# Performance work log

Hardware: AMD Instinct MI355X
Metric: run time of the kernel (lower is better)

Reference implementation:

```python
import jax, jax.numpy as jnp
import numpy as np

S, B, D, H, FF = 1024, 8, 512, 8, 2048
HD = D // H
ALPHA, BETA = 0.5, 0.5
EPS = 1e-5


def setup_inputs() -> dict:
    key = jax.random.key(0)
    ks = jax.random.split(key, 12)
    rn = lambda k, sh, sc=0.02: jax.random.normal(k, sh, dtype=jnp.float32) * sc
    ln = jnp.stack([jnp.ones(D), jnp.zeros(D), jnp.ones(D), jnp.zeros(D)]).astype(jnp.float32)
    return {
        "src": rn(ks[0], (S, B, D), 1.0),
        "src_depth": rn(ks[1], (S, B, D), 1.0),
        "pos": rn(ks[2], (S, B, D), 1.0),
        "attn_w_img": rn(ks[3], (4, D, D)),
        "attn_b_img": jnp.zeros((4, D), jnp.float32),
        "attn_w_dpt": rn(ks[4], (4, D, D)),
        "attn_b_dpt": jnp.zeros((4, D), jnp.float32),
        "ffn_w1_img": rn(ks[5], (FF, D)),
        "ffn_b1_img": jnp.zeros((FF,), jnp.float32),
        "ffn_w2_img": rn(ks[6], (D, FF)),
        "ffn_b2_img": jnp.zeros((D,), jnp.float32),
        "ffn_w1_dpt": rn(ks[7], (FF, D)),
        "ffn_b1_dpt": jnp.zeros((FF,), jnp.float32),
        "ffn_w2_dpt": rn(ks[8], (D, FF)),
        "ffn_b2_dpt": jnp.zeros((D,), jnp.float32),
        "ln_img": ln,
        "ln_dpt": ln,
    }


def _layer_norm(x, g, b):
    m = jnp.mean(x, axis=-1, keepdims=True)
    v = jnp.var(x, axis=-1, keepdims=True)  # biased, matches torch LayerNorm
    return (x - m) * jax.lax.rsqrt(v + EPS) * g + b


def _heads(t, W, b):  # [B,S,D] x [D,D] -> [B,H,S,hd]  (torch Linear: y = x W^T + b)
    y = jnp.einsum('bsd,ed->bse', t, W) + b
    return y.reshape(B, S, H, HD).transpose(0, 2, 1, 3)


def _forward(src, src_depth, pos, attn_w_img, attn_b_img, attn_w_dpt, attn_b_dpt,
             ffn_w1_img, ffn_b1_img, ffn_w2_img, ffn_b2_img,
             ffn_w1_dpt, ffn_b1_dpt, ffn_w2_dpt, ffn_b2_dpt, ln_img, ln_dpt):
    # seq-first -> batch-first
    x = src.transpose(1, 0, 2)        # [B,S,D]
    xd = src_depth.transpose(1, 0, 2)
    p = pos.transpose(1, 0, 2)
    qk_in = x + p                     # img stream: q = k = src + pos
    # depth stream: pos_depth is None in layer.forward -> no pos embed
    q = _heads(qk_in, attn_w_img[0], attn_b_img[0])
    k = _heads(qk_in, attn_w_img[1], attn_b_img[1])
    v = _heads(x, attn_w_img[2], attn_b_img[2])
    qd = _heads(xd, attn_w_dpt[0], attn_b_dpt[0])
    kd = _heads(xd, attn_w_dpt[1], attn_b_dpt[1])
    vd = _heads(xd, attn_w_dpt[2], attn_b_dpt[2])
    scale = 1.0 / np.sqrt(HD).astype(np.float32)
    a_img = jax.nn.softmax(jnp.einsum('bhld,bhsd->bhls', q, k) * scale, axis=-1)
    a_dpt = jax.nn.softmax(jnp.einsum('bhld,bhsd->bhls', qd, kd) * scale, axis=-1)
    sh_img = (1.0 - ALPHA) * a_img + ALPHA * a_dpt
    sh_dpt = (1.0 - BETA) * a_dpt + BETA * a_img
    o_img = jnp.einsum('bhls,bhsd->bhld', sh_img, v).transpose(0, 2, 1, 3).reshape(B, S, D)
    o_dpt = jnp.einsum('bhls,bhsd->bhld', sh_dpt, vd).transpose(0, 2, 1, 3).reshape(B, S, D)
    o_img = jnp.einsum('bsd,ed->bse', o_img, attn_w_img[3]) + attn_b_img[3]
    o_dpt = jnp.einsum('bsd,ed->bse', o_dpt, attn_w_dpt[3]) + attn_b_dpt[3]
    # img residual + LN + FFN + LN
    x = _layer_norm(x + o_img, ln_img[0], ln_img[1])
    ff = jnp.einsum('bsf,df->bsd',
                    jax.nn.relu(jnp.einsum('bsd,fd->bsf', x, ffn_w1_img) + ffn_b1_img),
                    ffn_w2_img) + ffn_b2_img
    x = _layer_norm(x + ff, ln_img[2], ln_img[3])
    # depth residual + LN + FFN + LN
    xd = _layer_norm(xd + o_dpt, ln_dpt[0], ln_dpt[1])
    ffd = jnp.einsum('bsf,df->bsd',
                     jax.nn.relu(jnp.einsum('bsd,fd->bsf', xd, ffn_w1_dpt) + ffn_b1_dpt),
                     ffn_w2_dpt) + ffn_b2_dpt
    xd = _layer_norm(xd + ffd, ln_dpt[2], ln_dpt[3])
    return x.transpose(1, 0, 2), xd.transpose(1, 0, 2)  # back to [S,B,D]


def reference(src, src_depth, pos, attn_w_img, attn_b_img, attn_w_dpt, attn_b_dpt,
              ffn_w1_img, ffn_b1_img, ffn_w2_img, ffn_b2_img,
              ffn_w1_dpt, ffn_b1_dpt, ffn_w2_dpt, ffn_b2_dpt, ln_img, ln_dpt):
    return _forward(src, src_depth, pos, attn_w_img, attn_b_img, attn_w_dpt, attn_b_dpt,
                    ffn_w1_img, ffn_b1_img, ffn_w2_img, ffn_b2_img,
                    ffn_w1_dpt, ffn_b1_dpt, ffn_w2_dpt, ffn_b2_dpt, ln_img, ln_dpt)
```

## Files before the change

### kernel.cpp

```cpp
#include <hip/hip_runtime.h>
#include <math.h>

#define S_  1024
#define B_  8
#define D_  512
#define H_  8
#define HD_ 64
#define FF_ 2048
#define M_  8192
#define DD_ (D_ * D_)

typedef __attribute__((ext_vector_type(8))) short short8;
typedef __attribute__((ext_vector_type(4))) float f32x4;

static __device__ __forceinline__ unsigned short f2bf(float x) {
  union { float f; unsigned int u; } v; v.f = x;
  unsigned int r = v.u + 0x7fff + ((v.u >> 16) & 1);
  return (unsigned short)(r >> 16);
}
static __device__ __forceinline__ float bf2f(unsigned short x) {
  union { unsigned int u; float f; } v; v.u = ((unsigned int)x) << 16;
  return v.f;
}
static __device__ __forceinline__ unsigned int pack_bf2(float a, float b) {
  union { float f; unsigned int u; } x, y; x.f = a; y.f = b;
  return ((x.u + 0x8000u) >> 16) | ((y.u + 0x8000u) & 0xffff0000u);
}
static __device__ __forceinline__ void gl_lds16(const unsigned short* g, unsigned short* l) {
  __builtin_amdgcn_global_load_lds((__attribute__((address_space(1))) void*)(g),
                                   (__attribute__((address_space(3))) void*)(l), 16, 0, 0);
}
static __device__ __forceinline__ int xcd_swz(int phys, int nwg) {
  int cpx = nwg >> 3;
  return (phys & 7) * cpx + (phys >> 3);
}

struct CvtJobs { const float* in[6]; unsigned short* out[6]; };
__global__ __launch_bounds__(256) void wcvt_kernel(CvtJobs j) {
  int job = blockIdx.y;
  int i = (blockIdx.x * 256 + threadIdx.x) * 4;
  float4 v = *(const float4*)(j.in[job] + i);
  unsigned short u[4] = {f2bf(v.x), f2bf(v.y), f2bf(v.z), f2bf(v.w)};
  *(uint2*)(j.out[job] + i) = *(const uint2*)u;
}

__global__ __launch_bounds__(256) void acvt_kernel(const float* __restrict__ src,
    const float* __restrict__ srcd, const float* __restrict__ pos,
    unsigned short* __restrict__ src16, unsigned short* __restrict__ srcd16,
    unsigned short* __restrict__ qkin16) {
  int job = blockIdx.y;
  int i = (blockIdx.x * 256 + threadIdx.x) * 4;
  const float* a = (job == 0) ? src : (job == 1) ? srcd : src;
  float4 v = *(const float4*)(a + i);
  if (job == 2) {
    float4 p = *(const float4*)(pos + i);
    v.x += p.x; v.y += p.y; v.z += p.z; v.w += p.w;
  }
  unsigned short* o = (job == 0) ? src16 : (job == 1) ? srcd16 : qkin16;
  unsigned short u[4] = {f2bf(v.x), f2bf(v.y), f2bf(v.z), f2bf(v.w)};
  *(uint2*)(o + i) = *(const uint2*)u;
}

static __device__ __forceinline__ void mgemm_body(
    const unsigned short* __restrict__ X, const unsigned short* __restrict__ W,
    const float* __restrict__ bias, const float* __restrict__ resf,
    const unsigned short* __restrict__ resb, unsigned short* __restrict__ Yb,
    float* __restrict__ Yf, int N, int K, int relu, int bx, int by,
    unsigned short* As, unsigned short* Bs)
{
  int tid = threadIdx.x;
  int lane = tid & 63, w = tid >> 6;
  int ml = lane & 15, g = lane >> 4;
  int wm = w >> 1, wn = w & 1;
  int m0 = by * 128, n0 = bx * 256;
  int mxs = (ml >> 1) & 3;

  int lrow = tid >> 2;
  int sg = (tid & 3) ^ ((lrow >> 1) & 3);
  const unsigned short* gA = X + (size_t)(m0 + lrow) * K + sg * 8;
  const unsigned short* gB = W + (size_t)(n0 + lrow) * K + sg * 8;
  unsigned short* lA = As + w * 512;
  unsigned short* lB = Bs + w * 512;

  f32x4 acc[4][8];
  #pragma unroll
  for (int i = 0; i < 4; i++)
    #pragma unroll
    for (int j = 0; j < 8; j++) acc[i][j] = (f32x4){0.f, 0.f, 0.f, 0.f};

  int NT = K >> 5;

  auto STAGE = [&](int buf, int kt) {
    const unsigned short* ga = gA + kt * 32;
    const unsigned short* gb = gB + kt * 32;
    unsigned short* la = lA + buf * 4096;
    unsigned short* lb = lB + buf * 8192;
    gl_lds16(ga, la);
    gl_lds16(ga + (size_t)64 * K, la + 2048);
    gl_lds16(gb, lb);
    gl_lds16(gb + (size_t)64 * K, lb + 2048);
    gl_lds16(gb + (size_t)128 * K, lb + 4096);
    gl_lds16(gb + (size_t)192 * K, lb + 6144);
  };

  STAGE(0, 0);
  __syncthreads();

  for (int kt = 0; kt < NT; kt++) {
    int cur = kt & 1;
    if (kt + 1 < NT) STAGE(cur ^ 1, kt + 1);

    const unsigned short* lAc = As + cur * 4096;
    const unsigned short* lBc = Bs + cur * 8192;
    short8 af[4], bfr[8];
    #pragma unroll
    for (int i = 0; i < 4; i++) {
      int r = wm * 64 + i * 16 + ml;
      af[i] = *(const short8*)&lAc[r * 32 + ((g ^ mxs) * 8)];
    }
    #pragma unroll
    for (int j = 0; j < 8; j++) {
      int r = wn * 128 + j * 16 + ml;
      bfr[j] = *(const short8*)&lBc[r * 32 + ((g ^ mxs) * 8)];
    }
    #pragma unroll
    for (int i = 0; i < 4; i++)
      #pragma unroll
      for (int j = 0; j < 8; j++)
        acc[i][j] = __builtin_amdgcn_mfma_f32_16x16x32_bf16(af[i], bfr[j], acc[i][j], 0, 0, 0);

    __syncthreads();
  }

  #pragma unroll
  for (int i = 0; i < 4; i++) {
    int grow = m0 + wm * 64 + i * 16 + g * 4;
    #pragma unroll
    for (int j = 0; j < 8; j++) {
      int gcol = n0 + wn * 128 + j * 16 + ml;
      float bv = bias[gcol];
      #pragma unroll
      for (int r = 0; r < 4; r++) {
        size_t idx = (size_t)(grow + r) * N + gcol;
        float v = acc[i][j][r] + bv;
        if (resf) v += resf[idx];
        if (resb) v += bf2f(resb[idx]);
        if (relu) v = fmaxf(v, 0.0f);
        if (Yb) Yb[idx] = f2bf(v);
        if (Yf) Yf[idx] = v;
      }
    }
  }
}

__global__ __launch_bounds__(256, 2) void qkv_kernel(
    const unsigned short* __restrict__ qkin, const unsigned short* __restrict__ src16,
    const unsigned short* __restrict__ srcd16,
    const unsigned short* __restrict__ w_i, const unsigned short* __restrict__ w_d,
    const float* __restrict__ bA_i, const float* __restrict__ bA_d,
    unsigned short* __restrict__ qkimg, unsigned short* __restrict__ vimg,
    unsigned short* __restrict__ dptqkv)
{
  __shared__ unsigned short As[2 * 128 * 32];
  __shared__ unsigned short Bs[2 * 256 * 32];
  int phys = blockIdx.x + 12 * blockIdx.y;
  int L = xcd_swz(phys, 12 * 64);
  int bx = L % 12, by = L / 12;
  if (bx < 4)
    mgemm_body(qkin, w_i, bA_i, nullptr, nullptr, qkimg, nullptr, 1024, 512, 0, bx, by, As, Bs);
  else if (bx < 6)
    mgemm_body(src16, w_i + 2 * DD_, bA_i + 1024, nullptr, nullptr, vimg, nullptr, 512, 512, 0, bx - 4, by, As, Bs);
  else
    mgemm_body(srcd16, w_d, bA_d, nullptr, nullptr, dptqkv, nullptr, 1536, 512, 0, bx - 6, by, As, Bs);
}

__global__ __launch_bounds__(256, 2) void pgemm_kernel(
    const unsigned short* __restrict__ X0, const unsigned short* __restrict__ X1,
    const unsigned short* __restrict__ W0, const unsigned short* __restrict__ W1,
    const float* __restrict__ b0, const float* __restrict__ b1,
    const float* __restrict__ rf0, const float* __restrict__ rf1,
    const unsigned short* __restrict__ rb0, const unsigned short* __restrict__ rb1,
    unsigned short* __restrict__ Y0, unsigned short* __restrict__ Y1,
    int N, int K, int relu)
{
  __shared__ unsigned short As[2 * 128 * 32];
  __shared__ unsigned short Bs[2 * 256 * 32];
  int nbx = gridDim.x;
  int nwg = nbx * 64 * 2;
  int phys = blockIdx.x + nbx * (blockIdx.y + 64 * blockIdx.z);
  int L = xcd_swz(phys, nwg);
  int bx = L % nbx; int rem = L / nbx;
  int by = rem % 64; int z = rem / 64;
  mgemm_body(z ? X1 : X0, z ? W1 : W0, z ? b1 : b0, z ? rf1 : rf0,
             z ? rb1 : rb0, z ? Y1 : Y0, nullptr, N, K, relu,
             bx, by, As, Bs);
}

__global__ __launch_bounds__(256) void vtrans_kernel(
    const unsigned short* __restrict__ v0, int ld0, unsigned short* __restrict__ vt0,
    const unsigned short* __restrict__ v1, int ld1, unsigned short* __restrict__ vt1)
{
  __shared__ unsigned short tile[64][72];
  const unsigned short* v = blockIdx.z ? v1 : v0;
  unsigned short* vt = blockIdx.z ? vt1 : vt0;
  int ld = blockIdx.z ? ld1 : ld0;
  int bh = blockIdx.y, b = bh >> 3, h = bh & 7;
  int s0 = blockIdx.x * 64;
  int tid = threadIdx.x;
  #pragma unroll
  for (int t = 0; t < 2; t++) {
    int idx = t * 256 + tid;
    int i = idx >> 3, c8 = (idx & 7) * 8;
    *(uint4*)&tile[i][c8] =
        *(const uint4*)(v + ((size_t)(s0 + i) * B_ + b) * ld + h * HD_ + c8);
  }
  __syncthreads();
  int hd = tid >> 2, j0 = (tid & 3) * 16;
  unsigned short tmp[16];
  #pragma unroll
  for (int j = 0; j < 16; j++) tmp[j] = tile[j0 + j][hd];
  unsigned short* dst = vt + ((size_t)bh * HD_ + hd) * S_ + s0 + j0;
  *(uint4*)(dst) = *(const uint4*)&tmp[0];
  *(uint4*)(dst + 8) = *(const uint4*)&tmp[8];
}

__global__ __launch_bounds__(256) void ln16_kernel(
    const unsigned short* __restrict__ X0, const unsigned short* __restrict__ X1,
    unsigned short* __restrict__ Yb0, unsigned short* __restrict__ Yb1,
    float* __restrict__ Yf0, float* __restrict__ Yf1,
    const float* __restrict__ gb0, const float* __restrict__ gb1)
{
  int row = blockIdx.x, tid = threadIdx.x;
  int strm = row >> 13, r = row & 8191;
  const unsigned short* X = strm ? X1 : X0;
  unsigned short* Yb = strm ? Yb1 : Yb0;
  float* Yf = strm ? Yf1 : Yf0;
  const float* gb = strm ? gb1 : gb0;

  ushort2 xv = *(const ushort2*)(X + (size_t)r * D_ + 2 * tid);
  float v0 = bf2f(xv.x), v1 = bf2f(xv.y);
  float s = v0 + v1, q = v0 * v0 + v1 * v1;
  #pragma unroll
  for (int msk = 1; msk < 64; msk <<= 1) {
    s += __shfl_xor(s, msk);
    q += __shfl_xor(q, msk);
  }
  __shared__ float ss[4], qs[4];
  int wid = tid >> 6;
  if ((tid & 63) == 0) { ss[wid] = s; qs[wid] = q; }
  __syncthreads();
  s = ss[0] + ss[1] + ss[2] + ss[3];
  q = qs[0] + qs[1] + qs[2] + qs[3];
  float mean = s * (1.0f / D_);
  float var  = q * (1.0f / D_) - mean * mean;
  float inv  = rsqrtf(var + 1e-5f);
  float2 gg = *(const float2*)(gb + 2 * tid);
  float2 bb = *(const float2*)(gb + 512 + 2 * tid);
  float o0 = (v0 - mean) * inv * gg.x + bb.x;
  float o1 = (v1 - mean) * inv * gg.y + bb.y;
  if (Yb) {
    unsigned short u[2] = {f2bf(o0), f2bf(o1)};
    *(unsigned int*)(Yb + (size_t)r * D_ + 2 * tid) = *(const unsigned int*)u;
  }
  if (Yf) {
    float2 o; o.x = o0; o.y = o1;
    *(float2*)(Yf + (size_t)r * D_ + 2 * tid) = o;
  }
}

__global__ __launch_bounds__(256, 2) void attn_kernel(
    const unsigned short* __restrict__ Qi, const unsigned short* __restrict__ Ki, int ldi,
    const unsigned short* __restrict__ Vti,
    const unsigned short* __restrict__ Qd, const unsigned short* __restrict__ Kd, int ldd,
    const unsigned short* __restrict__ Vtd,
    unsigned short* __restrict__ oi, unsigned short* __restrict__ od)
{
  __shared__ __align__(16) unsigned short Kls[2][64 * 64];
  __shared__ __align__(16) unsigned short Vls[2][64 * 64];
  __shared__ __align__(16) unsigned short Pl[4][2][16 * 72];

  int tid = threadIdx.x;
  int phys = blockIdx.x + 8 * blockIdx.y;
  int L = xcd_swz(phys, 8 * 64);
  int bh = L >> 3, b = bh >> 3, h = bh & 7;
  int q0 = (L & 7) * 128;
  int lane = tid & 63, w = tid >> 6;
  int ml = lane & 15, g = lane >> 4;
  int mx = ml & 7;

  short8 qf[2][2][2];
  #pragma unroll
  for (int t = 0; t < 2; t++) {
    size_t tok = (size_t)(q0 + w * 32 + t * 16 + ml) * B_ + b;
    const unsigned short* qa_i = Qi + tok * ldi + h * HD_ + g * 8;
    const unsigned short* qa_d = Qd + tok * ldd + h * HD_ + g * 8;
    qf[t][0][0] = *(const short8*)(qa_i);  qf[t][0][1] = *(const short8*)(qa_i + 32);
    qf[t][1][0] = *(const short8*)(qa_d);  qf[t][1][1] = *(const short8*)(qa_d + 32);
  }

  int srow = lane >> 3;
  int chg = (lane & 7) ^ srow;
  const unsigned short* gbase; size_t s1, s2; unsigned short* lbase;
  if (w == 0)      { gbase = Ki  + ((size_t)srow * B_ + b) * ldi + h * HD_ + chg * 8; s1 = (size_t)B_ * ldi; s2 = s1; lbase = &Kls[0][0]; }
  else if (w == 1) { gbase = Kd  + ((size_t)srow * B_ + b) * ldd + h * HD_ + chg * 8; s1 = (size_t)B_ * ldd; s2 = s1; lbase = &Kls[1][0]; }
  else if (w == 2) { gbase = Vti + (size_t)bh * HD_ * S_ + (size_t)srow * S_ + chg * 8; s1 = S_; s2 = 1; lbase = &Vls[0][0]; }
  else             { gbase = Vtd + (size_t)bh * HD_ * S_ + (size_t)srow * S_ + chg * 8; s1 = S_; s2 = 1; lbase = &Vls[1][0]; }

  f32x4 acc4[2][4][4];
  #pragma unroll
  for (int t = 0; t < 2; t++)
    #pragma unroll
    for (int cb = 0; cb < 4; cb++)
      #pragma unroll
      for (int n = 0; n < 4; n++) acc4[t][cb][n] = (f32x4){0.f, 0.f, 0.f, 0.f};
  float lI[2] = {0.f, 0.f}, lD[2] = {0.f, 0.f};
  const float scale = 0.125f;

  for (int kt = 0; kt < S_ / 64; kt++) {
    int k0 = kt * 64;
    __syncthreads();
    {
      const unsigned short* gp = gbase + (size_t)k0 * s2;
      #pragma unroll
      for (int rr = 0; rr < 8; rr++)
        gl_lds16(gp + (size_t)rr * 8 * s1, lbase + rr * 512);
    }
    __syncthreads();

    #pragma unroll
    for (int t = 0; t < 2; t++) {
      #pragma unroll
      for (int st = 0; st < 2; st++) {
        float* ls = st ? &lD[t] : &lI[t];
        const unsigned short* Kt = &Kls[st][0];
        #pragma unroll
        for (int n = 0; n < 4; n++) {
          int rbase = (n * 16 + ml) * 64;
          short8 kf0 = *(const short8*)&Kt[rbase + ((g ^ mx) * 8)];
          short8 kf1 = *(const short8*)&Kt[rbase + (((g + 4) ^ mx) * 8)];
          f32x4 a = (f32x4){0.f, 0.f, 0.f, 0.f};
          a = __builtin_amdgcn_mfma_f32_16x16x32_bf16(kf0, qf[t][st][0], a, 0, 0, 0);
          a = __builtin_amdgcn_mfma_f32_16x16x32_bf16(kf1, qf[t][st][1], a, 0, 0, 0);
          float p0 = __expf(a[0] * scale), p1 = __expf(a[1] * scale);
          float p2 = __expf(a[2] * scale), p3 = __expf(a[3] * scale);
          *ls += (p0 + p1) + (p2 + p3);
          uint2 pk; pk.x = pack_bf2(p0, p1); pk.y = pack_bf2(p2, p3);
          *(uint2*)&Pl[w][st][ml * 72 + n * 16 + g * 4] = pk;
        }
      }
      #pragma unroll
      for (int c = 0; c < 2; c++) {
        short8 pI = *(const short8*)&Pl[w][0][ml * 72 + g * 8 + c * 32];
        short8 pD = *(const short8*)&Pl[w][1][ml * 72 + g * 8 + c * 32];
        #pragma unroll
        for (int n = 0; n < 4; n++) {
          int rbase = (n * 16 + ml) * 64;
          int sc = (((g + 4 * c) ^ mx)) * 8;
          short8 vI = *(const short8*)&Vls[0][rbase + sc];
          short8 vD = *(const short8*)&Vls[1][rbase + sc];
          acc4[t][0][n] = __builtin_amdgcn_mfma_f32_16x16x32_bf16(pI, vI, acc4[t][0][n], 0, 0, 0);
          acc4[t][1][n] = __builtin_amdgcn_mfma_f32_16x16x32_bf16(pD, vI, acc4[t][1][n], 0, 0, 0);
          acc4[t][2][n] = __builtin_amdgcn_mfma_f32_16x16x32_bf16(pI, vD, acc4[t][2][n], 0, 0, 0);
          acc4[t][3][n] = __builtin_amdgcn_mfma_f32_16x16x32_bf16(pD, vD, acc4[t][3][n], 0, 0, 0);
        }
      }
    }
  }

  #pragma unroll
  for (int t = 0; t < 2; t++) {
    lI[t] += __shfl_xor(lI[t], 16);  lI[t] += __shfl_xor(lI[t], 32);
    lD[t] += __shfl_xor(lD[t], 16);  lD[t] += __shfl_xor(lD[t], 32);
  }
  #pragma unroll
  for (int t = 0; t < 2; t++) {
    float invI = 1.0f / lI[t], invD = 1.0f / lD[t];
    #pragma unroll
    for (int r = 0; r < 4; r++) {
      float iI = __shfl(invI, g * 4 + r, 16);
      float iD = __shfl(invD, g * 4 + r, 16);
      int qrow = q0 + w * 32 + t * 16 + g * 4 + r;
      size_t ob = ((size_t)qrow * B_ + b) * D_ + h * HD_;
      #pragma unroll
      for (int n = 0; n < 4; n++) {
        oi[ob + n * 16 + ml] = f2bf(0.5f * (acc4[t][0][n][r] * iI + acc4[t][1][n][r] * iD));
        od[ob + n * 16 + ml] = f2bf(0.5f * (acc4[t][3][n][r] * iD + acc4[t][2][n][r] * iI));
      }
    }
  }
}

extern "C" void kernel_launch(void* const* d_in, const int* in_sizes, int n_in,
                              void* d_out, int out_size, void* d_ws, size_t ws_size,
                              hipStream_t stream) {
  const float* src  = (const float*)d_in[0];
  const float* srcd = (const float*)d_in[1];
  const float* pos  = (const float*)d_in[2];
  const float* wA_i = (const float*)d_in[3];
  const float* bA_i = (const float*)d_in[4];
  const float* wA_d = (const float*)d_in[5];
  const float* bA_d = (const float*)d_in[6];
  const float* w1_i = (const float*)d_in[7];
  const float* b1_i = (const float*)d_in[8];
  const float* w2_i = (const float*)d_in[9];
  const float* b2_i = (const float*)d_in[10];
  const float* w1_d = (const float*)d_in[11];
  const float* b1_d = (const float*)d_in[12];
  const float* w2_d = (const float*)d_in[13];
  const float* b2_d = (const float*)d_in[14];
  const float* ln_i = (const float*)d_in[15];
  const float* ln_d = (const float*)d_in[16];

  float* out = (float*)d_out;
  unsigned short* u = (unsigned short*)d_ws;
  const size_t T4 = (size_t)M_ * D_;
  const size_t WSZ = (size_t)FF_ * D_;

  unsigned short* src16  = u;
  unsigned short* srcd16 = u + T4;
  unsigned short* qkimg  = u + 2 * T4;
  unsigned short* vimg   = u + 4 * T4;
  unsigned short* dptqkv = u + 5 * T4;
  unsigned short* w_i16  = u + 8 * T4;
  unsigned short* w_d16  = w_i16 + WSZ;
  unsigned short* w1i16  = w_d16 + WSZ;
  unsigned short* w2i16  = w1i16 + WSZ;
  unsigned short* w1d16  = w2i16 + WSZ;
  unsigned short* w2d16  = w1d16 + WSZ;
  unsigned short* t16_i  = w2d16 + WSZ;
  unsigned short* t16_d  = t16_i + T4;
  unsigned short* x16_i  = t16_d + T4;
  unsigned short* x16_d  = x16_i + T4;
  unsigned short* vt_i   = src16;
  unsigned short* vt_d   = srcd16;
  unsigned short* h16_i  = u;
  unsigned short* h16_d  = u + 4 * T4;
  unsigned short* qkin16 = (unsigned short*)out;
  unsigned short* oi16   = (unsigned short*)out;
  unsigned short* od16   = (unsigned short*)out + T4;

  dim3 blk(256);

  CvtJobs cj;
  cj.in[0] = wA_i; cj.out[0] = w_i16;
  cj.in[1] = wA_d; cj.out[1] = w_d16;
  cj.in[2] = w1_i; cj.out[2] = w1i16;
  cj.in[3] = w2_i; cj.out[3] = w2i16;
  cj.in[4] = w1_d; cj.out[4] = w1d16;
  cj.in[5] = w2_d; cj.out[5] = w2d16;
  wcvt_kernel<<<dim3(1024, 6), blk, 0, stream>>>(cj);
  acvt_kernel<<<dim3(4096, 3), blk, 0, stream>>>(src, srcd, pos, src16, srcd16, qkin16);

  qkv_kernel<<<dim3(12, 64), blk, 0, stream>>>(qkin16, src16, srcd16, w_i16, w_d16,
                                               bA_i, bA_d, qkimg, vimg, dptqkv);
  vtrans_kernel<<<dim3(16, 64, 2), blk, 0, stream>>>(vimg, 512, vt_i, dptqkv + 1024, 1536, vt_d);

  attn_kernel<<<dim3(S_ / 128, B_ * H_), blk, 0, stream>>>(
      qkimg, qkimg + 512, 1024, vt_i, dptqkv, dptqkv + 512, 1536, vt_d, oi16, od16);

  pgemm_kernel<<<dim3(2, 64, 2), blk, 0, stream>>>(
      oi16, od16, w_i16 + 3 * DD_, w_d16 + 3 * DD_, bA_i + 1536, bA_d + 1536,
      src, srcd, nullptr, nullptr, t16_i, t16_d, 512, 512, 0);
  ln16_kernel<<<2 * M_, blk, 0, stream>>>(t16_i, t16_d, x16_i, x16_d,
                                          nullptr, nullptr, ln_i, ln_d);
  pgemm_kernel<<<dim3(8, 64, 2), blk, 0, stream>>>(
      x16_i, x16_d, w1i16, w1d16, b1_i, b1_d,
      nullptr, nullptr, nullptr, nullptr, h16_i, h16_d, 2048, 512, 1);
  pgemm_kernel<<<dim3(2, 64, 2), blk, 0, stream>>>(
      h16_i, h16_d, w2i16, w2d16, b2_i, b2_d,
      nullptr, nullptr, x16_i, x16_d, t16_i, t16_d, 512, 2048, 0);
  ln16_kernel<<<2 * M_, blk, 0, stream>>>(t16_i, t16_d, nullptr, nullptr,
                                          out, out + T4, ln_i + 2 * D_, ln_d + 2 * D_);
}
```

Before: 483.9 us.

## Retile GEMMs to 256-row tiles with 512 threads and 64-wide K steps

```diff
diff --git a/kernel.cpp b/kernel.cpp
--- a/kernel.cpp
+++ b/kernel.cpp
@@ -61,46 +61,46 @@
   *(uint2*)(o + i) = *(const uint2*)u;
 }
 
-static __device__ __forceinline__ void mgemm_body(
+template <int NR>
+static __device__ __forceinline__ void mgemm8_body(
     const unsigned short* __restrict__ X, const unsigned short* __restrict__ W,
     const float* __restrict__ bias, const float* __restrict__ resf,
     const unsigned short* __restrict__ resb, unsigned short* __restrict__ Yb,
-    float* __restrict__ Yf, int N, int K, int relu, int bx, int by,
+    int N, int K, int relu, int bx, int by,
     unsigned short* As, unsigned short* Bs)
 {
   int tid = threadIdx.x;
   int lane = tid & 63, w = tid >> 6;
   int ml = lane & 15, g = lane >> 4;
-  int wm = w >> 1, wn = w & 1;
-  int m0 = by * 128, n0 = bx * 256;
-  int mxs = (ml >> 1) & 3;
-
-  int lrow = tid >> 2;
-  int sg = (tid & 3) ^ ((lrow >> 1) & 3);
-  const unsigned short* gA = X + (size_t)(m0 + lrow) * K + sg * 8;
-  const unsigned short* gB = W + (size_t)(n0 + lrow) * K + sg * 8;
+  int wm = w >> 2, wn = w & 3;
+  int m0 = by * 256, n0 = bx * (NR * 64);
+
+  int lrow = tid >> 3;
+  int gcolc = ((tid & 7) ^ (lrow & 7)) * 8;
+  const unsigned short* gA = X + (size_t)(m0 + lrow) * K + gcolc;
+  const unsigned short* gB = W + (size_t)(n0 + lrow) * K + gcolc;
   unsigned short* lA = As + w * 512;
   unsigned short* lB = Bs + w * 512;
 
-  f32x4 acc[4][8];
-  #pragma unroll
-  for (int i = 0; i < 4; i++)
-    #pragma unroll
-    for (int j = 0; j < 8; j++) acc[i][j] = (f32x4){0.f, 0.f, 0.f, 0.f};
-
-  int NT = K >> 5;
+  f32x4 acc[8][NR];
+  #pragma unroll
+  for (int i = 0; i < 8; i++)
+    #pragma unroll
+    for (int j = 0; j < NR; j++) acc[i][j] = (f32x4){0.f, 0.f, 0.f, 0.f};
+
+  int NT = K >> 6;
 
   auto STAGE = [&](int buf, int kt) {
-    const unsigned short* ga = gA + kt * 32;
-    const unsigned short* gb = gB + kt * 32;
-    unsigned short* la = lA + buf * 4096;
-    unsigned short* lb = lB + buf * 8192;
-    gl_lds16(ga, la);
-    gl_lds16(ga + (size_t)64 * K, la + 2048);
-    gl_lds16(gb, lb);
-    gl_lds16(gb + (size_t)64 * K, lb + 2048);
-    gl_lds16(gb + (size_t)128 * K, lb + 4096);
-    gl_lds16(gb + (size_t)192 * K, lb + 6144);
+    const unsigned short* ga = gA + kt * 64;
+    const unsigned short* gb = gB + kt * 64;
+    unsigned short* la = lA + buf * 16384;
+    unsigned short* lb = lB + buf * (NR * 4096);
+    #pragma unroll
+    for (int q = 0; q < 4; q++)
+      gl_lds16(ga + (size_t)q * 64 * K, la + q * 4096);
+    #pragma unroll
+    for (int q = 0; q < NR; q++)
+      gl_lds16(gb + (size_t)q * 64 * K, lb + q * 4096);
   };
 
   STAGE(0, 0);
@@ -110,34 +110,36 @@
     int cur = kt & 1;
     if (kt + 1 < NT) STAGE(cur ^ 1, kt + 1);
 
-    const unsigned short* lAc = As + cur * 4096;
-    const unsigned short* lBc = Bs + cur * 8192;
-    short8 af[4], bfr[8];
-    #pragma unroll
-    for (int i = 0; i < 4; i++) {
-      int r = wm * 64 + i * 16 + ml;
-      af[i] = *(const short8*)&lAc[r * 32 + ((g ^ mxs) * 8)];
+    const unsigned short* lAc = As + cur * 16384;
+    const unsigned short* lBc = Bs + cur * (NR * 4096);
+    #pragma unroll
+    for (int ks = 0; ks < 2; ks++) {
+      short8 af[8], bfr[NR];
+      #pragma unroll
+      for (int i = 0; i < 8; i++) {
+        int r = wm * 128 + i * 16 + ml;
+        af[i] = *(const short8*)&lAc[r * 64 + (((ks * 4 + g) ^ (r & 7)) * 8)];
+      }
+      #pragma unroll
+      for (int j = 0; j < NR; j++) {
+        int r = wn * (NR * 16) + j * 16 + ml;
+        bfr[j] = *(const short8*)&lBc[r * 64 + (((ks * 4 + g) ^ (r & 7)) * 8)];
+      }
+      #pragma unroll
+      for (int i = 0; i < 8; i++)
+        #pragma unroll
+        for (int j = 0; j < NR; j++)
+          acc[i][j] = __builtin_amdgcn_mfma_f32_16x16x32_bf16(af[i], bfr[j], acc[i][j], 0, 0, 0);
     }
-    #pragma unroll
-    for (int j = 0; j < 8; j++) {
-      int r = wn * 128 + j * 16 + ml;
-      bfr[j] = *(const short8*)&lBc[r * 32 + ((g ^ mxs) * 8)];
-    }
-    #pragma unroll
-    for (int i = 0; i < 4; i++)
-      #pragma unroll
-      for (int j = 0; j < 8; j++)
-        acc[i][j] = __builtin_amdgcn_mfma_f32_16x16x32_bf16(af[i], bfr[j], acc[i][j], 0, 0, 0);
-
     __syncthreads();
   }
 
   #pragma unroll
-  for (int i = 0; i < 4; i++) {
-    int grow = m0 + wm * 64 + i * 16 + g * 4;
-    #pragma unroll
-    for (int j = 0; j < 8; j++) {
-      int gcol = n0 + wn * 128 + j * 16 + ml;
+  for (int i = 0; i < 8; i++) {
+    int grow = m0 + wm * 128 + i * 16 + g * 4;
+    #pragma unroll
+    for (int j = 0; j < NR; j++) {
+      int gcol = n0 + wn * (NR * 16) + j * 16 + ml;
       float bv = bias[gcol];
       #pragma unroll
       for (int r = 0; r < 4; r++) {
@@ -146,14 +148,13 @@
         if (resf) v += resf[idx];
         if (resb) v += bf2f(resb[idx]);
         if (relu) v = fmaxf(v, 0.0f);
-        if (Yb) Yb[idx] = f2bf(v);
-        if (Yf) Yf[idx] = v;
+        Yb[idx] = f2bf(v);
       }
     }
   }
 }
 
-__global__ __launch_bounds__(256, 2) void qkv_kernel(
+__global__ __launch_bounds__(512, 2) void qkv_kernel(
     const unsigned short* __restrict__ qkin, const unsigned short* __restrict__ src16,
     const unsigned short* __restrict__ srcd16,
     const unsigned short* __restrict__ w_i, const unsigned short* __restrict__ w_d,
@@ -161,20 +162,21 @@
     unsigned short* __restrict__ qkimg, unsigned short* __restrict__ vimg,
     unsigned short* __restrict__ dptqkv)
 {
-  __shared__ unsigned short As[2 * 128 * 32];
-  __shared__ unsigned short Bs[2 * 256 * 32];
+  __shared__ unsigned short As[2 * 256 * 64];
+  __shared__ unsigned short Bs[2 * 256 * 64];
   int phys = blockIdx.x + 12 * blockIdx.y;
-  int L = xcd_swz(phys, 12 * 64);
+  int L = xcd_swz(phys, 12 * 32);
   int bx = L % 12, by = L / 12;
   if (bx < 4)
-    mgemm_body(qkin, w_i, bA_i, nullptr, nullptr, qkimg, nullptr, 1024, 512, 0, bx, by, As, Bs);
+    mgemm8_body<4>(qkin, w_i, bA_i, nullptr, nullptr, qkimg, 1024, 512, 0, bx, by, As, Bs);
   else if (bx < 6)
-    mgemm_body(src16, w_i + 2 * DD_, bA_i + 1024, nullptr, nullptr, vimg, nullptr, 512, 512, 0, bx - 4, by, As, Bs);
+    mgemm8_body<4>(src16, w_i + 2 * DD_, bA_i + 1024, nullptr, nullptr, vimg, 512, 512, 0, bx - 4, by, As, Bs);
   else
-    mgemm_body(srcd16, w_d, bA_d, nullptr, nullptr, dptqkv, nullptr, 1536, 512, 0, bx - 6, by, As, Bs);
-}
-
-__global__ __launch_bounds__(256, 2) void pgemm_kernel(
+    mgemm8_body<4>(srcd16, w_d, bA_d, nullptr, nullptr, dptqkv, 1536, 512, 0, bx - 6, by, As, Bs);
+}
+
+template <int NR>
+__global__ __launch_bounds__(512, 2) void pgemm_kernel(
     const unsigned short* __restrict__ X0, const unsigned short* __restrict__ X1,
     const unsigned short* __restrict__ W0, const unsigned short* __restrict__ W1,
     const float* __restrict__ b0, const float* __restrict__ b1,
@@ -183,17 +185,16 @@
     unsigned short* __restrict__ Y0, unsigned short* __restrict__ Y1,
     int N, int K, int relu)
 {
-  __shared__ unsigned short As[2 * 128 * 32];
-  __shared__ unsigned short Bs[2 * 256 * 32];
+  __shared__ unsigned short As[2 * 256 * 64];
+  __shared__ unsigned short Bs[2 * NR * 64 * 64];
   int nbx = gridDim.x;
-  int nwg = nbx * 64 * 2;
-  int phys = blockIdx.x + nbx * (blockIdx.y + 64 * blockIdx.z);
+  int nwg = nbx * 32 * 2;
+  int phys = blockIdx.x + nbx * (blockIdx.y + 32 * blockIdx.z);
   int L = xcd_swz(phys, nwg);
   int bx = L % nbx; int rem = L / nbx;
-  int by = rem % 64; int z = rem / 64;
-  mgemm_body(z ? X1 : X0, z ? W1 : W0, z ? b1 : b0, z ? rf1 : rf0,
-             z ? rb1 : rb0, z ? Y1 : Y0, nullptr, N, K, relu,
-             bx, by, As, Bs);
+  int by = rem % 32; int z = rem / 32;
+  mgemm8_body<NR>(z ? X1 : X0, z ? W1 : W0, z ? b1 : b0, z ? rf1 : rf0,
+                  z ? rb1 : rb0, z ? Y1 : Y0, N, K, relu, bx, by, As, Bs);
 }
 
 __global__ __launch_bounds__(256) void vtrans_kernel(
@@ -440,6 +441,7 @@
   unsigned short* od16   = (unsigned short*)out + T4;
 
   dim3 blk(256);
+  dim3 blk512(512);
 
   CvtJobs cj;
   cj.in[0] = wA_i; cj.out[0] = w_i16;
@@ -451,22 +453,22 @@
   wcvt_kernel<<<dim3(1024, 6), blk, 0, stream>>>(cj);
   acvt_kernel<<<dim3(4096, 3), blk, 0, stream>>>(src, srcd, pos, src16, srcd16, qkin16);
 
-  qkv_kernel<<<dim3(12, 64), blk, 0, stream>>>(qkin16, src16, srcd16, w_i16, w_d16,
-                                               bA_i, bA_d, qkimg, vimg, dptqkv);
+  qkv_kernel<<<dim3(12, 32), blk512, 0, stream>>>(qkin16, src16, srcd16, w_i16, w_d16,
+                                                  bA_i, bA_d, qkimg, vimg, dptqkv);
   vtrans_kernel<<<dim3(16, 64, 2), blk, 0, stream>>>(vimg, 512, vt_i, dptqkv + 1024, 1536, vt_d);
 
   attn_kernel<<<dim3(S_ / 128, B_ * H_), blk, 0, stream>>>(
       qkimg, qkimg + 512, 1024, vt_i, dptqkv, dptqkv + 512, 1536, vt_d, oi16, od16);
 
-  pgemm_kernel<<<dim3(2, 64, 2), blk, 0, stream>>>(
+  pgemm_kernel<2><<<dim3(4, 32, 2), blk512, 0, stream>>>(
       oi16, od16, w_i16 + 3 * DD_, w_d16 + 3 * DD_, bA_i + 1536, bA_d + 1536,
       src, srcd, nullptr, nullptr, t16_i, t16_d, 512, 512, 0);
   ln16_kernel<<<2 * M_, blk, 0, stream>>>(t16_i, t16_d, x16_i, x16_d,
                                           nullptr, nullptr, ln_i, ln_d);
-  pgemm_kernel<<<dim3(8, 64, 2), blk, 0, stream>>>(
+  pgemm_kernel<4><<<dim3(8, 32, 2), blk512, 0, stream>>>(
       x16_i, x16_d, w1i16, w1d16, b1_i, b1_d,
       nullptr, nullptr, nullptr, nullptr, h16_i, h16_d, 2048, 512, 1);
-  pgemm_kernel<<<dim3(2, 64, 2), blk, 0, stream>>>(
+  pgemm_kernel<2><<<dim3(4, 32, 2), blk512, 0, stream>>>(
       h16_i, h16_d, w2i16, w2d16, b2_i, b2_d,
       nullptr, nullptr, x16_i, x16_d, t16_i, t16_d, 512, 2048, 0);
   ln16_kernel<<<2 * M_, blk, 0, stream>>>(t16_i, t16_d, nullptr, nullptr,
```

Result: faster. 440.0 us (-9.1%).
